# Performance work log

Hardware: AMD Instinct MI355X
Metric: run time of the kernel (lower is better)

The kernel has to match this reference:

```python
import jax, jax.numpy as jnp
import numpy as np

N, D_IN, D_OUT, E = 4096, 4096, 4096, 8

def setup_inputs() -> dict:
    key = jax.random.key(0)
    k1, k2, k3 = jax.random.split(key, 3)
    scale_in = 1.0 / np.sqrt(D_IN)
    x = jax.random.normal(k1, (N, D_IN), dtype=jnp.float32)
    gate_w = jax.random.normal(k2, (D_IN, E), dtype=jnp.float32) * scale_in
    gate_b = jnp.zeros((E,), dtype=jnp.float32)
    expert_w = jax.random.normal(k3, (E, D_IN, D_OUT), dtype=jnp.float32) * scale_in
    expert_b = jnp.zeros((E, D_OUT), dtype=jnp.float32)
    return {"x": x, "gate_w": gate_w, "gate_b": gate_b,
            "expert_w": expert_w, "expert_b": expert_b}

def reference(x, gate_w, gate_b, expert_w, expert_b):
    # gate scores: [N, E]
    gate = jax.nn.softmax(x @ gate_w + gate_b, axis=-1)
    # all experts run on every token: [E, N, D_OUT]
    expert_out = jnp.einsum('nd,edr->enr', x, expert_w) + expert_b[:, None, :]
    # gate-weighted combine: [N, D_OUT]
    out = jnp.einsum('ne,enr->nr', gate, expert_out)
    return out
```

## Files before the change

kernel.cpp:

```cpp
#include <hip/hip_runtime.h>
#include <hip/hip_bf16.h>


typedef __attribute__((ext_vector_type(8))) short short8;
typedef __attribute__((ext_vector_type(4))) float f32x4;

#define NROWS 4096
#define DIN   4096
#define DOUT  4096
#define NEXP  8
#define KTOT  (NEXP * DIN)

__device__ __forceinline__ unsigned short f2b(float f) {
  unsigned int u = __float_as_uint(f);
  u += 0x7FFFu + ((u >> 16) & 1u);
  return (unsigned short)(u >> 16);
}

__device__ __forceinline__ void gload_lds16(const unsigned short* g, unsigned short* l) {
  __builtin_amdgcn_global_load_lds(
      (const __attribute__((address_space(1))) unsigned int*)(unsigned long long)g,
      (__attribute__((address_space(3))) unsigned int*)(unsigned int)(unsigned long long)l,
      16, 0, 0);
}

__global__ __launch_bounds__(256) void gate_kernel(const float* __restrict__ x,
                                                   const float* __restrict__ gw,
                                                   const float* __restrict__ gb,
                                                   float* __restrict__ g,
                                                   unsigned short* __restrict__ xb) {
  __shared__ float red[4][8];
  const int n = blockIdx.x, t = threadIdx.x;
  const int lane = t & 63, w = t >> 6;
  float a[8] = {0, 0, 0, 0, 0, 0, 0, 0};
  #pragma unroll
  for (int it = 0; it < DIN / 1024; ++it) {
    const int d = (it * 256 + t) * 4;
    float4 xv = *(const float4*)(x + (size_t)n * DIN + d);
    ushort4 p;
    p.x = f2b(xv.x); p.y = f2b(xv.y); p.z = f2b(xv.z); p.w = f2b(xv.w);
    *(ushort4*)(xb + (size_t)n * DIN + d) = p;
    const float xs[4] = {xv.x, xv.y, xv.z, xv.w};
    #pragma unroll
    for (int q = 0; q < 4; ++q) {
      const float4* gwp = (const float4*)(gw + (size_t)(d + q) * 8);
      float4 w0 = gwp[0], w1 = gwp[1];
      a[0] += xs[q] * w0.x; a[1] += xs[q] * w0.y; a[2] += xs[q] * w0.z; a[3] += xs[q] * w0.w;
      a[4] += xs[q] * w1.x; a[5] += xs[q] * w1.y; a[6] += xs[q] * w1.z; a[7] += xs[q] * w1.w;
    }
  }
  #pragma unroll
  for (int off = 32; off; off >>= 1)
    #pragma unroll
    for (int e = 0; e < 8; ++e) a[e] += __shfl_xor(a[e], off);
  if (lane == 0)
    #pragma unroll
    for (int e = 0; e < 8; ++e) red[w][e] = a[e];
  __syncthreads();
  if (t == 0) {
    float l[8], m = -1e30f, ssum = 0.f;
    for (int e = 0; e < 8; ++e) {
      l[e] = red[0][e] + red[1][e] + red[2][e] + red[3][e] + gb[e];
      m = fmaxf(m, l[e]);
    }
    for (int e = 0; e < 8; ++e) { l[e] = expf(l[e] - m); ssum += l[e]; }
    for (int e = 0; e < 8; ++e) g[(size_t)n * 8 + e] = l[e] / ssum;
  }
}

__global__ __launch_bounds__(256) void transpose_w(const float* __restrict__ W,
                                                   unsigned short* __restrict__ bt) {
  __shared__ unsigned short tile[64 * 64];
  const int t = threadIdx.x;
  const int k0 = blockIdx.x * 64, r0 = blockIdx.y * 64;
  #pragma unroll
  for (int i = 0; i < 4; ++i) {
    int lin = i * 256 + t;
    int kr = lin >> 4;
    int G = lin & 15;
    float4 v = *(const float4*)(W + (size_t)(k0 + kr) * 4096 + r0 + G * 4);
    int slot = G ^ (kr & 15) ^ ((kr >> 4) & 3);
    ushort4 p;
    p.x = f2b(v.x); p.y = f2b(v.y); p.z = f2b(v.z); p.w = f2b(v.w);
    *(ushort4*)&tile[kr * 64 + slot * 4] = p;
  }
  __syncthreads();
  #pragma unroll
  for (int i = 0; i < 2; ++i) {
    int lin = i * 256 + t;
    int rr = lin >> 3;
    int kc = (lin & 7) * 8;
    unsigned short buf[8];
    #pragma unroll
    for (int j = 0; j < 8; ++j) {
      int k = kc + j;
      int slot = (rr >> 2) ^ (k & 15) ^ ((k >> 4) & 3);
      buf[j] = tile[k * 64 + slot * 4 + (rr & 3)];
    }
    *(uint4*)(bt + (size_t)(r0 + rr) * KTOT + k0 + kc) = *(uint4*)buf;
  }
}

#define BM 256
#define BN 256
#define BKK 32
#define NTILES (KTOT / BKK)
#define SLOT_SH 8192

__global__ __launch_bounds__(512, 2) void gemm_moe(const unsigned short* __restrict__ xb,
                                                   const unsigned short* __restrict__ bt,
                                                   const float* __restrict__ gate,
                                                   const float* __restrict__ eb,
                                                   float* __restrict__ out) {
  __shared__ alignas(16) unsigned short sA[4 * SLOT_SH];
  __shared__ alignas(16) unsigned short sB[4 * SLOT_SH];
  __shared__ float sG[256 * 8];
  __shared__ float sBias[8 * 256];

  const int t = threadIdx.x;
  const int lane = t & 63;
  const int w = t >> 6;
  const int wm = w >> 2;
  const int wn = w & 3;

  const int bid = blockIdx.x;
  const int wg = (bid & 7) * 32 + (bid >> 3);
  const int tn = wg >> 4;
  const int tm = wg & 15;
  const int row0 = tm * BM;
  const int col0 = tn * BN;

  #pragma unroll
  for (int i = 0; i < 4; ++i) {
    int lin = i * 512 + t;
    sG[lin] = gate[(size_t)row0 * 8 + lin];
    sBias[lin] = eb[(size_t)(lin >> 8) * DOUT + col0 + (lin & 255)];
  }

  const int mrow = lane & 15;
  const int quad = lane >> 4;
  const int rs = (quad ^ ((mrow >> 1) & 3)) * 8;

  const int srow = w * 16 + (lane >> 2);
  const int sg0 = (lane & 3) ^ ((srow >> 1) & 3);
  const int sg1 = (lane & 3) ^ (((srow + 128) >> 1) & 3);

  f32x4 acc[8][4];
  #pragma unroll
  for (int i = 0; i < 8; ++i)
    #pragma unroll
    for (int j = 0; j < 4; ++j) acc[i][j] = (f32x4){0.f, 0.f, 0.f, 0.f};

  auto stageA = [&](int T) {
    const int s = T & 3;
    const int kA = (T * BKK) & (DIN - 1);
    gload_lds16(xb + (size_t)(row0 + srow) * DIN + kA + sg0 * 8,
                &sA[s * SLOT_SH + (w * 64) * 8]);
    gload_lds16(xb + (size_t)(row0 + 128 + srow) * DIN + kA + sg1 * 8,
                &sA[s * SLOT_SH + (512 + w * 64) * 8]);
  };
  auto stageB = [&](int T) {
    const int s = T & 3;
    const int kB = T * BKK;
    gload_lds16(bt + (size_t)(col0 + srow) * KTOT + kB + sg0 * 8,
                &sB[s * SLOT_SH + (w * 64) * 8]);
    gload_lds16(bt + (size_t)(col0 + 128 + srow) * KTOT + kB + sg1 * 8,
                &sB[s * SLOT_SH + (512 + w * 64) * 8]);
  };

  stageA(0); stageB(0);
  stageA(1); stageB(1);
  asm volatile("s_waitcnt vmcnt(4)" ::: "memory");
  __builtin_amdgcn_s_barrier();

  for (int T = 0; T < NTILES; ++T) {
    const int s = T & 3;
    const unsigned short* sAs = &sA[s * SLOT_SH];
    const unsigned short* sBs = &sB[s * SLOT_SH];

    short8 af0[4], bf[4];
    #pragma unroll
    for (int i = 0; i < 4; ++i)
      af0[i] = *(const short8*)&sAs[(wm * 128 + i * 16 + mrow) * 32 + rs];
    #pragma unroll
    for (int j = 0; j < 4; ++j)
      bf[j] = *(const short8*)&sBs[(wn * 64 + j * 16 + mrow) * 32 + rs];
    if (T < NTILES - 2) stageA(T + 2);
    __builtin_amdgcn_s_barrier();
    asm volatile("s_waitcnt lgkmcnt(0)" ::: "memory");
    __builtin_amdgcn_s_setprio(1);
    #pragma unroll
    for (int i = 0; i < 4; ++i)
      #pragma unroll
      for (int j = 0; j < 4; ++j)
        acc[i][j] = __builtin_amdgcn_mfma_f32_16x16x32_bf16(af0[i], bf[j], acc[i][j], 0, 0, 0);
    __builtin_amdgcn_s_setprio(0);
    __builtin_amdgcn_s_barrier();

    short8 af1[4];
    #pragma unroll
    for (int i = 0; i < 4; ++i)
      af1[i] = *(const short8*)&sAs[(wm * 128 + (4 + i) * 16 + mrow) * 32 + rs];
    if (T < NTILES - 2) stageB(T + 2);
    __builtin_amdgcn_s_barrier();
    asm volatile("s_waitcnt lgkmcnt(0)" ::: "memory");
    __builtin_amdgcn_s_setprio(1);
    #pragma unroll
    for (int i = 0; i < 4; ++i)
      #pragma unroll
      for (int j = 0; j < 4; ++j)
        acc[4 + i][j] = __builtin_amdgcn_mfma_f32_16x16x32_bf16(af1[i], bf[j], acc[4 + i][j], 0, 0, 0);
    __builtin_amdgcn_s_setprio(0);

    if (T < NTILES - 1) {
      if (T < NTILES - 2) asm volatile("s_waitcnt vmcnt(4)" ::: "memory");
      else                asm volatile("s_waitcnt vmcnt(0)" ::: "memory");
      __builtin_amdgcn_s_barrier();

      if ((T & 127) == 127) {
        const int e = T >> 7;
        #pragma unroll
        for (int i = 0; i < 8; ++i) {
          #pragma unroll
          for (int r = 0; r < 4; ++r) {
            const int row_l = wm * 128 + i * 16 + quad * 4 + r;
            const float sc = sG[row_l * 8 + e] / sG[row_l * 8 + e + 1];
            #pragma unroll
            for (int j = 0; j < 4; ++j) acc[i][j][r] *= sc;
          }
        }
      }
    }
  }

  #pragma unroll
  for (int i = 0; i < 8; ++i) {
    #pragma unroll
    for (int r = 0; r < 4; ++r) {
      const int row_l = wm * 128 + i * 16 + quad * 4 + r;
      float gv[8];
      #pragma unroll
      for (int e = 0; e < 8; ++e) gv[e] = sG[row_l * 8 + e];
      #pragma unroll
      for (int j = 0; j < 4; ++j) {
        const int col_l = wn * 64 + j * 16 + mrow;
        float bias = 0.f;
        #pragma unroll
        for (int e = 0; e < 8; ++e) bias += gv[e] * sBias[e * 256 + col_l];
        out[(size_t)(row0 + row_l) * DOUT + col0 + col_l] = acc[i][j][r] * gv[7] + bias;
      }
    }
  }
}

__global__ __launch_bounds__(256) void moe_fallback(const float* __restrict__ x,
                                                    const float* __restrict__ gw,
                                                    const float* __restrict__ gb,
                                                    const float* __restrict__ W,
                                                    const float* __restrict__ eb,
                                                    float* __restrict__ out) {
  __shared__ float sX[64][33];
  __shared__ float sW[32][65];
  __shared__ float sLog[64][8];
  __shared__ float sGate[64][8];
  const int t = threadIdx.x;
  const int r0 = blockIdx.y * 64, c0 = blockIdx.x * 64;

  const int grow = t & 63, epair = t >> 6;
  float lg0 = gb[2 * epair], lg1 = gb[2 * epair + 1];
  for (int d0 = 0; d0 < DIN; d0 += 32) {
    for (int i = 0; i < 8; ++i) {
      int lin = i * 256 + t, rr = lin >> 5, cc = lin & 31;
      sX[rr][cc] = x[(size_t)(r0 + rr) * DIN + d0 + cc];
    }
    __syncthreads();
    for (int dd = 0; dd < 32; ++dd) {
      float xv = sX[grow][dd];
      lg0 += xv * gw[(size_t)(d0 + dd) * 8 + 2 * epair];
      lg1 += xv * gw[(size_t)(d0 + dd) * 8 + 2 * epair + 1];
    }
    __syncthreads();
  }
  sLog[grow][2 * epair] = lg0;
  sLog[grow][2 * epair + 1] = lg1;
  __syncthreads();
  if (t < 64) {
    float m = -1e30f, s = 0.f, ex[8];
    for (int e = 0; e < 8; ++e) m = fmaxf(m, sLog[t][e]);
    for (int e = 0; e < 8; ++e) { ex[e] = expf(sLog[t][e] - m); s += ex[e]; }
    for (int e = 0; e < 8; ++e) sGate[t][e] = ex[e] / s;
  }
  __syncthreads();

  const int tr = t >> 4, tc = t & 15;
  float acc[4][4] = {};
  for (int e = 0; e < NEXP; ++e) {
    float part[4][4] = {};
    for (int d0 = 0; d0 < DIN; d0 += 32) {
      for (int i = 0; i < 8; ++i) {
        int lin = i * 256 + t, rr = lin >> 5, cc = lin & 31;
        sX[rr][cc] = x[(size_t)(r0 + rr) * DIN + d0 + cc];
      }
      for (int i = 0; i < 8; ++i) {
        int lin = i * 256 + t, dd = lin >> 6, cc = lin & 63;
        sW[dd][cc] = W[(size_t)e * DIN * DOUT + (size_t)(d0 + dd) * DOUT + c0 + cc];
      }
      __syncthreads();
      for (int dd = 0; dd < 32; ++dd) {
        float xa[4], wb[4];
        for (int i = 0; i < 4; ++i) xa[i] = sX[tr + 16 * i][dd];
        for (int j = 0; j < 4; ++j) wb[j] = sW[dd][tc + 16 * j];
        for (int i = 0; i < 4; ++i)
          for (int j = 0; j < 4; ++j) part[i][j] += xa[i] * wb[j];
      }
      __syncthreads();
    }
    for (int i = 0; i < 4; ++i) {
      float g = sGate[tr + 16 * i][e];
      for (int j = 0; j < 4; ++j)
        acc[i][j] += g * (part[i][j] + eb[(size_t)e * DOUT + c0 + tc + 16 * j]);
    }
  }
  for (int i = 0; i < 4; ++i)
    for (int j = 0; j < 4; ++j)
      out[(size_t)(r0 + tr + 16 * i) * DOUT + c0 + tc + 16 * j] = acc[i][j];
}

extern "C" void kernel_launch(void* const* d_in, const int* in_sizes, int n_in,
                              void* d_out, int out_size, void* d_ws, size_t ws_size,
                              hipStream_t stream) {
  const float* x  = (const float*)d_in[0];
  const float* gw = (const float*)d_in[1];
  const float* gb = (const float*)d_in[2];
  const float* W  = (const float*)d_in[3];
  const float* eb = (const float*)d_in[4];
  float* out = (float*)d_out;

  const size_t sz_xb = (size_t)NROWS * DIN * 2;
  const size_t sz_bt = (size_t)DOUT * KTOT * 2;
  const size_t sz_g  = (size_t)NROWS * 8 * 4;
  const size_t need = sz_xb + sz_bt + sz_g;

  if (ws_size >= need) {
    unsigned short* xb = (unsigned short*)d_ws;
    unsigned short* bt = (unsigned short*)((char*)d_ws + sz_xb);
    float* gate = (float*)((char*)d_ws + sz_xb + sz_bt);
    gate_kernel<<<NROWS, 256, 0, stream>>>(x, gw, gb, gate, xb);
    transpose_w<<<dim3(KTOT / 64, DOUT / 64), 256, 0, stream>>>(W, bt);
    gemm_moe<<<(NROWS / BM) * (DOUT / BN), 512, 0, stream>>>(xb, bt, gate, eb, out);
  } else {
    moe_fallback<<<dim3(DOUT / 64, NROWS / 64), 256, 0, stream>>>(x, gw, gb, W, eb, out);
  }
}
```

Before: 1.804 ms.

## Store transposed expert weights in K-tiled blocks and merge MFMA half-phases

The weight-transpose kernel now writes bf16 weights in a K-tiled layout: each 32-wide K slice for 256 output columns is laid out contiguously, and it processes 256 columns per block with a new LDS swizzle. The GEMM B staging reads from this contiguous tile layout, so B global loads touch dense memory instead of rows strided by the full K. The main loop also drops the split into two half-phases with intermediate barriers. It now issues both A and B prefetches up front, loads all eight A fragments and runs all 32 MFMAs in one block. This cuts barrier and wait overhead, at the cost of more live VGPRs and less interleaving between LDS reads and MFMAs.

```diff
diff --git a/kernel.cpp b/kernel.cpp
--- a/kernel.cpp
+++ b/kernel.cpp
@@ -70,34 +70,36 @@
 
 __global__ __launch_bounds__(256) void transpose_w(const float* __restrict__ W,
                                                    unsigned short* __restrict__ bt) {
-  __shared__ unsigned short tile[64 * 64];
+  __shared__ unsigned short tile[64 * 256];
   const int t = threadIdx.x;
-  const int k0 = blockIdx.x * 64, r0 = blockIdx.y * 64;
-  #pragma unroll
-  for (int i = 0; i < 4; ++i) {
+  const int k0 = blockIdx.x * 64, r0 = blockIdx.y * 256;
+  #pragma unroll
+  for (int i = 0; i < 16; ++i) {
     int lin = i * 256 + t;
-    int kr = lin >> 4;
-    int G = lin & 15;
-    float4 v = *(const float4*)(W + (size_t)(k0 + kr) * 4096 + r0 + G * 4);
-    int slot = G ^ (kr & 15) ^ ((kr >> 4) & 3);
+    int kr = lin >> 6;
+    int gg = lin & 63;
+    float4 v = *(const float4*)(W + (size_t)(k0 + kr) * 4096 + r0 + gg * 4);
+    int slot = gg ^ (kr & 31);
     ushort4 p;
     p.x = f2b(v.x); p.y = f2b(v.y); p.z = f2b(v.z); p.w = f2b(v.w);
-    *(ushort4*)&tile[kr * 64 + slot * 4] = p;
+    *(ushort4*)&tile[kr * 256 + slot * 4] = p;
   }
   __syncthreads();
   #pragma unroll
-  for (int i = 0; i < 2; ++i) {
+  for (int i = 0; i < 8; ++i) {
     int lin = i * 256 + t;
-    int rr = lin >> 3;
-    int kc = (lin & 7) * 8;
+    int kc = (lin & 3) * 8;
+    int c  = (lin >> 2) & 255;
+    int Tl = lin >> 10;
     unsigned short buf[8];
     #pragma unroll
     for (int j = 0; j < 8; ++j) {
-      int k = kc + j;
-      int slot = (rr >> 2) ^ (k & 15) ^ ((k >> 4) & 3);
-      buf[j] = tile[k * 64 + slot * 4 + (rr & 3)];
-    }
-    *(uint4*)(bt + (size_t)(r0 + rr) * KTOT + k0 + kc) = *(uint4*)buf;
+      int k = Tl * 32 + kc + j;
+      int slot = (c >> 2) ^ (k & 31);
+      buf[j] = tile[k * 256 + slot * 4 + (c & 3)];
+    }
+    size_t T = (size_t)(blockIdx.x * 2 + Tl);
+    *(uint4*)(bt + (T * 4096 + r0 + c) * 32 + kc) = *(uint4*)buf;
   }
 }
 
@@ -161,10 +163,10 @@
   };
   auto stageB = [&](int T) {
     const int s = T & 3;
-    const int kB = T * BKK;
-    gload_lds16(bt + (size_t)(col0 + srow) * KTOT + kB + sg0 * 8,
+    const unsigned short* base = bt + ((size_t)T * 4096 + col0) * 32;
+    gload_lds16(base + (size_t)srow * 32 + sg0 * 8,
                 &sB[s * SLOT_SH + (w * 64) * 8]);
-    gload_lds16(bt + (size_t)(col0 + 128 + srow) * KTOT + kB + sg1 * 8,
+    gload_lds16(base + (size_t)(128 + srow) * 32 + sg1 * 8,
                 &sB[s * SLOT_SH + (512 + w * 64) * 8]);
   };
 
@@ -178,38 +180,22 @@
     const unsigned short* sAs = &sA[s * SLOT_SH];
     const unsigned short* sBs = &sB[s * SLOT_SH];
 
-    short8 af0[4], bf[4];
-    #pragma unroll
-    for (int i = 0; i < 4; ++i)
-      af0[i] = *(const short8*)&sAs[(wm * 128 + i * 16 + mrow) * 32 + rs];
+    if (T < NTILES - 2) { stageA(T + 2); stageB(T + 2); }
+
+    short8 af[8], bf[4];
+    #pragma unroll
+    for (int i = 0; i < 8; ++i)
+      af[i] = *(const short8*)&sAs[(wm * 128 + i * 16 + mrow) * 32 + rs];
     #pragma unroll
     for (int j = 0; j < 4; ++j)
       bf[j] = *(const short8*)&sBs[(wn * 64 + j * 16 + mrow) * 32 + rs];
-    if (T < NTILES - 2) stageA(T + 2);
-    __builtin_amdgcn_s_barrier();
-    asm volatile("s_waitcnt lgkmcnt(0)" ::: "memory");
+
     __builtin_amdgcn_s_setprio(1);
     #pragma unroll
-    for (int i = 0; i < 4; ++i)
+    for (int i = 0; i < 8; ++i)
       #pragma unroll
       for (int j = 0; j < 4; ++j)
-        acc[i][j] = __builtin_amdgcn_mfma_f32_16x16x32_bf16(af0[i], bf[j], acc[i][j], 0, 0, 0);
-    __builtin_amdgcn_s_setprio(0);
-    __builtin_amdgcn_s_barrier();
-
-    short8 af1[4];
-    #pragma unroll
-    for (int i = 0; i < 4; ++i)
-      af1[i] = *(const short8*)&sAs[(wm * 128 + (4 + i) * 16 + mrow) * 32 + rs];
-    if (T < NTILES - 2) stageB(T + 2);
-    __builtin_amdgcn_s_barrier();
-    asm volatile("s_waitcnt lgkmcnt(0)" ::: "memory");
-    __builtin_amdgcn_s_setprio(1);
-    #pragma unroll
-    for (int i = 0; i < 4; ++i)
-      #pragma unroll
-      for (int j = 0; j < 4; ++j)
-        acc[4 + i][j] = __builtin_amdgcn_mfma_f32_16x16x32_bf16(af1[i], bf[j], acc[4 + i][j], 0, 0, 0);
+        acc[i][j] = __builtin_amdgcn_mfma_f32_16x16x32_bf16(af[i], bf[j], acc[i][j], 0, 0, 0);
     __builtin_amdgcn_s_setprio(0);
 
     if (T < NTILES - 1) {
@@ -346,7 +332,7 @@
     unsigned short* bt = (unsigned short*)((char*)d_ws + sz_xb);
     float* gate = (float*)((char*)d_ws + sz_xb + sz_bt);
     gate_kernel<<<NROWS, 256, 0, stream>>>(x, gw, gb, gate, xb);
-    transpose_w<<<dim3(KTOT / 64, DOUT / 64), 256, 0, stream>>>(W, bt);
+    transpose_w<<<dim3(KTOT / 64, DOUT / 256), 256, 0, stream>>>(W, bt);
     gemm_moe<<<(NROWS / BM) * (DOUT / BN), 512, 0, stream>>>(xb, bt, gate, eb, out);
   } else {
     moe_fallback<<<dim3(DOUT / 64, NROWS / 64), 256, 0, stream>>>(x, gw, gb, W, eb, out);
```

Result: faster. 1.724 ms (-4.4%).
